# Optimization experiments

Measured on AMD Instinct MI355X. Metric: run time of the kernel, lower is better.

## Reference

```python
import jax, jax.numpy as jnp
import numpy as np

SLEN, BSZ, D_MODEL, N_HEAD, D_HEAD, PROJ_DIM = 2048, 2, 1024, 16, 64, 256
LN_EPS = 1e-5
PRIME_EPS = 1e-4


def setup_inputs() -> dict:
    key = jax.random.key(0)
    ks = jax.random.split(key, 4)
    h = jax.random.normal(ks[0], (SLEN, BSZ, D_MODEL), jnp.float32)
    W_qkvb = jax.random.normal(ks[1], (D_MODEL, N_HEAD * (3 * D_HEAD + 1)), jnp.float32) * (D_MODEL ** -0.5)
    W_o = jax.random.normal(ks[2], (N_HEAD * D_HEAD, D_MODEL), jnp.float32) * ((N_HEAD * D_HEAD) ** -0.5)
    ln_gamma = jnp.ones((D_MODEL,), jnp.float32)
    ln_beta = jnp.zeros((D_MODEL,), jnp.float32)
    # orthogonal random matrix (d_head, proj_dim): blocks of orthonormal cols, rows scaled to norm sqrt(d)
    rng = np.random.default_rng(0)
    blocks = []
    for _ in range(PROJ_DIM // D_HEAD):
        qm, _ = np.linalg.qr(rng.standard_normal((D_HEAD, D_HEAD)))
        blocks.append(qm)
    pm = np.concatenate(blocks, axis=1) * np.sqrt(D_HEAD)
    proj_matrix = jnp.asarray(pm, jnp.float32)  # (d_head, proj_dim)
    return {"h": h, "W_qkvb": W_qkvb, "W_o": W_o, "ln_gamma": ln_gamma,
            "ln_beta": ln_beta, "proj_matrix": proj_matrix}


def prime(x, pm):
    # FAVOR+ hyperbolic softmax-kernel features. x: (B,H,L,d), pm: (d,m) -> (B,H,L,2m)
    d = x.shape[-1]
    m = pm.shape[-1]
    xn = x * (d ** -0.25)
    proj = jnp.einsum('bhld,dm->bhlm', xn, pm)
    hnorm = 0.5 * jnp.sum(xn * xn, axis=-1, keepdims=True)
    feat = jnp.concatenate([jnp.exp(proj - hnorm), jnp.exp(-proj - hnorm)], axis=-1)
    return ((2 * m) ** -0.5) * (feat + PRIME_EPS)


def layer_norm(x, gamma, beta):
    mu = jnp.mean(x, axis=-1, keepdims=True)
    var = jnp.mean(jnp.square(x - mu), axis=-1, keepdims=True)
    return (x - mu) * jax.lax.rsqrt(var + LN_EPS) * gamma + beta


def reference(h, W_qkvb, W_o, ln_gamma, ln_beta, proj_matrix):
    slen, bsz, _ = h.shape
    qkvb = (h @ W_qkvb).reshape(slen, bsz, N_HEAD, 3 * D_HEAD + 1)
    q, k, v, hb = jnp.split(qkvb, [D_HEAD, 2 * D_HEAD, 3 * D_HEAD], axis=-1)
    hb = jax.nn.sigmoid(hb)
    # (L,B,H,*) -> (B,H,L,*)
    q = q.transpose(1, 2, 0, 3)
    k = k.transpose(1, 2, 0, 3)
    v = v.transpose(1, 2, 0, 3)
    hb = hb.transpose(1, 2, 0, 3)
    qp = prime(q, proj_matrix)
    kp = prime(k, proj_matrix)
    kp = kp / kp.sum(-1, keepdims=True)
    qp = qp / qp.sum(-1, keepdims=True)
    # time-major for the scan: (L,B,H,*)
    qpT = qp.transpose(2, 0, 1, 3)
    kpT = kp.transpose(2, 0, 1, 3)
    vT = v.transpose(2, 0, 1, 3)
    hbT = hb.transpose(2, 0, 1, 3)
    W0 = jnp.zeros((bsz, N_HEAD, 2 * PROJ_DIM, D_HEAD), h.dtype)

    def step(W, inp):
        qt, kt, vt, bt = inp  # (B,H,2m),(B,H,2m),(B,H,d),(B,H,1)
        v_old = jnp.einsum('bhpd,bhp->bhd', W, kt)
        W = W + jnp.einsum('bhp,bhd->bhpd', kt, bt * (vt - v_old))
        out = jnp.einsum('bhpd,bhp->bhd', W, qt)
        return W, out

    _, outs = jax.lax.scan(step, W0, (qpT, kpT, vT, hbT))  # outs: (L,B,H,d)
    scale = D_HEAD ** -0.5
    layer_out = (scale * outs).reshape(slen, bsz, N_HEAD * D_HEAD)
    attn_out = layer_out @ W_o
    return layer_norm(h + attn_out, ln_gamma, ln_beta)
```

## Files before the change

### kernel.cpp

```cpp
#include <hip/hip_runtime.h>
#include <hip/hip_bf16.h>

#define LSEQ   2048
#define BSZN   2
#define DMODEL 1024
#define NHEAD  16
#define DH     64
#define MPROJ  256
#define PF     512
#define CHK    64
#define NCHK   32
#define BHN    32
#define NQKV   3088
#define NQPAD  3200

typedef __hip_bfloat16 bf16;
typedef short bf16x8 __attribute__((ext_vector_type(8)));
typedef float f32x4 __attribute__((ext_vector_type(4)));

#define MFMA(a, b, c) __builtin_amdgcn_mfma_f32_16x16x32_bf16(a, b, c, 0, 0, 0)

#define UNP(u, a, b) { a = __uint_as_float((unsigned)(u) << 16); b = __uint_as_float((unsigned)(u) & 0xffff0000u); }

static __device__ __forceinline__ float b2f(bf16 x) {
  unsigned short us = *(unsigned short*)&x;
  return __uint_as_float((unsigned)us << 16);
}
static __device__ __forceinline__ bf16 f2b(float x) { return __float2bfloat16(x); }
static __device__ __forceinline__ unsigned pkbf(float a, float b) {
  bf16 x = __float2bfloat16(a), y = __float2bfloat16(b);
  return ((unsigned)(*(unsigned short*)&y) << 16) | (unsigned)(*(unsigned short*)&x);
}

static __device__ __forceinline__ void gl_lds16(const void* gsrc, void* ldst) {
  __builtin_amdgcn_global_load_lds(
      (const __attribute__((address_space(1))) unsigned int*)gsrc,
      (__attribute__((address_space(3))) unsigned int*)ldst, 16, 0, 0);
}

#define MEMFENCE asm volatile("" ::: "memory")
#define WAITV(n) asm volatile("s_waitcnt vmcnt(" #n ")" ::: "memory")
#define WAITLGKM asm volatile("s_waitcnt lgkmcnt(0)" ::: "memory")
#define BARRIER() __builtin_amdgcn_s_barrier()

__global__ __launch_bounds__(256)
void k_cvth(const float* __restrict__ h, bf16* __restrict__ hbf)
{
  const int gt = blockIdx.x * 256 + threadIdx.x;
  const int r = gt >> 7, ug = gt & 127;
  const int grp = ug >> 3, u = ug & 7;
  const float4 f0 = *(const float4*)&h[(size_t)r * 1024 + grp * 64 + u * 8];
  const float4 f1 = *(const float4*)&h[(size_t)r * 1024 + grp * 64 + u * 8 + 4];
  uint4 o;
  o.x = pkbf(f0.x, f0.y); o.y = pkbf(f0.z, f0.w);
  o.z = pkbf(f1.x, f1.y); o.w = pkbf(f1.z, f1.w);
  *(uint4*)&hbf[(size_t)r * 1024 + grp * 64 + ((u ^ (r & 7)) << 3)] = o;
}

__global__ __launch_bounds__(256)
void k_cvtw(const float* __restrict__ W, bf16* __restrict__ WT, int nsrc)
{
  __shared__ float sT[64][65];
  const int tid = threadIdx.x;
  const int n0 = blockIdx.x * 64, k0 = blockIdx.y * 64;
#pragma unroll
  for (int j = 0; j < 16; j++) {
    const int e = j * 256 + tid;
    const int r = e >> 6, c = e & 63;
    sT[r][c] = (n0 + c < nsrc) ? W[(size_t)(k0 + r) * nsrc + n0 + c] : 0.f;
  }
  __syncthreads();
#pragma unroll
  for (int j = 0; j < 2; j++) {
    const int uid = j * 256 + tid;
    const int rp = uid >> 3, u = uid & 7;
    uint4 o;
    o.x = pkbf(sT[u * 8 + 0][rp], sT[u * 8 + 1][rp]);
    o.y = pkbf(sT[u * 8 + 2][rp], sT[u * 8 + 3][rp]);
    o.z = pkbf(sT[u * 8 + 4][rp], sT[u * 8 + 5][rp]);
    o.w = pkbf(sT[u * 8 + 6][rp], sT[u * 8 + 7][rp]);
    *(uint4*)&WT[(size_t)(n0 + rp) * 1024 + k0 + ((u ^ (rp & 7)) << 3)] = o;
  }
}

__global__ __launch_bounds__(256)
void k_cvtpm(const float* __restrict__ pm, bf16* __restrict__ pmThi,
             bf16* __restrict__ pmTlo)
{
  const int n = threadIdx.x;
  float v[64];
#pragma unroll
  for (int d = 0; d < 64; d++) v[d] = pm[d * MPROJ + n] * 0.35355339059327373f;
  const int key = n & 7;
#pragma unroll
  for (int u = 0; u < 8; u++) {
    unsigned hi[4], lo[4];
#pragma unroll
    for (int j = 0; j < 4; j++) {
      const float a = v[u * 8 + j * 2], b = v[u * 8 + j * 2 + 1];
      const bf16 ah = f2b(a), bh_ = f2b(b);
      const float ar = a - b2f(ah), br = b - b2f(bh_);
      hi[j] = ((unsigned)(*(const unsigned short*)&bh_) << 16) | (unsigned)(*(const unsigned short*)&ah);
      const bf16 al = f2b(ar), bl = f2b(br);
      lo[j] = ((unsigned)(*(const unsigned short*)&bl) << 16) | (unsigned)(*(const unsigned short*)&al);
    }
    *(uint4*)&pmThi[(size_t)n * 64 + ((u ^ key) << 3)] = make_uint4(hi[0], hi[1], hi[2], hi[3]);
    *(uint4*)&pmTlo[(size_t)n * 64 + ((u ^ key) << 3)] = make_uint4(lo[0], lo[1], lo[2], lo[3]);
  }
}

#define GEMM_STAGE(Abase, Bbase, kt, b) {                                      \
  const size_t kb = (size_t)(kt) * 128;           \
  _Pragma("unroll")                                                            \
  for (int j = 0; j < 4; j++) {                                                \
    const int row = (w * 4 + j) * 8 + (lane >> 3);                             \
    gl_lds16((const char*)(Abase) + (size_t)(m0 + row) * 2048 + kb + (lane & 7) * 16, \
             &sA[b][(w * 4 + j) * 1024]);                                      \
  }                                                                            \
  _Pragma("unroll")                                                            \
  for (int j = 0; j < 4; j++) {                                                \
    const int row = (w * 4 + j) * 8 + (lane >> 3);                             \
    gl_lds16((const char*)(Bbase) + (size_t)(n0 + row) * 2048 + kb + (lane & 7) * 16, \
             &sB[b][(w * 4 + j) * 1024]);                                      \
  } }

#define GEMM_COMPUTE(b) {                                                      \
  _Pragma("unroll")                                                            \
  for (int ks = 0; ks < 2; ks++) {                                             \
    bf16x8 af[4], bfr[4];                                                      \
    _Pragma("unroll")                                                          \
    for (int f = 0; f < 4; f++) {                                              \
      const int row = wm * 64 + f * 16 + l16;                                  \
      af[f] = *(const bf16x8*)&sA[b][row * 128 + (((ks * 4 + lg) ^ xs) << 4)]; \
    }                                                                          \
    _Pragma("unroll")                                                          \
    for (int f = 0; f < 4; f++) {                                              \
      const int row = wn * 64 + f * 16 + l16;                                  \
      bfr[f] = *(const bf16x8*)&sB[b][row * 128 + (((ks * 4 + lg) ^ xs) << 4)]; \
    }                                                                          \
    _Pragma("unroll")                                                          \
    for (int fm = 0; fm < 4; fm++)                                             \
      _Pragma("unroll")                                                        \
      for (int fn = 0; fn < 4; fn++)                                           \
        acc[fm][fn] = MFMA(af[fm], bfr[fn], acc[fm][fn]);                      \
  } }

#define GEMM_PREAMBLE                                                          \
  __shared__ __align__(16) char sA[2][16384];                                  \
  __shared__ __align__(16) char sB[2][16384];                                  \
  const int tid = threadIdx.x, w = tid >> 6, lane = tid & 63;                  \
  const int l16 = lane & 15, lg = lane >> 4;                                   \
  const int wm = w >> 1, wn = w & 1;                                           \
  const int m0 = blockIdx.y * 128, n0 = blockIdx.x * 128;                      \
  const int xs = l16 & 7;                                                      \
  f32x4 acc[4][4];                                                             \
  _Pragma("unroll")                                                            \
  for (int i = 0; i < 4; i++)                                                  \
    _Pragma("unroll")                                                          \
    for (int j = 0; j < 4; j++) acc[i][j] = (f32x4){0.f, 0.f, 0.f, 0.f};

__global__ __launch_bounds__(256, 2)
void k_gemm_qkvb(const bf16* __restrict__ A, const bf16* __restrict__ B,
                 bf16* __restrict__ qh, bf16* __restrict__ kh,
                 bf16* __restrict__ vh, float* __restrict__ bbuf)
{
  GEMM_PREAMBLE
  GEMM_STAGE(A, B, 0, 0);
  __syncthreads();
  for (int kt = 0; kt < 16; kt++) {
    const int b = kt & 1;
    if (kt < 15) GEMM_STAGE(A, B, kt + 1, b ^ 1);
    GEMM_COMPUTE(b);
    __syncthreads();
  }
#pragma unroll
  for (int fm = 0; fm < 4; fm++)
#pragma unroll
    for (int fn = 0; fn < 4; fn++)
#pragma unroll
      for (int reg = 0; reg < 4; reg++) {
        const int m = m0 + wm * 64 + fm * 16 + lg * 4 + reg;
        const int n = n0 + wn * 64 + fn * 16 + l16;
        if (n >= NQKV) continue;
        const float v = acc[fm][fn][reg];
        const int l = m >> 1, bidx = m & 1;
        const int hd = n / 193;
        const int rem = n - hd * 193;
        const int bhi = bidx * NHEAD + hd;
        const size_t o = ((size_t)bhi * LSEQ + l) * DH;
        if (rem < 64) {
          const int d = rem;
          qh[o + ((((d >> 3) ^ (l & 7)) << 3) | (d & 7))] = f2b(v);
        } else if (rem < 128) {
          const int d = rem - 64;
          kh[o + ((((d >> 3) ^ (l & 7)) << 3) | (d & 7))] = f2b(v);
        } else if (rem < 192) {
          vh[o + rem - 128] = f2b(v);
        } else {
          bbuf[(size_t)bhi * LSEQ + l] = 1.f / (1.f + __expf(-v));
        }
      }
}

__global__ __launch_bounds__(256, 2)
void k_gemm_out(const bf16* __restrict__ A, const bf16* __restrict__ B,
                const float* __restrict__ h, float* __restrict__ ao)
{
  GEMM_PREAMBLE
  GEMM_STAGE(A, B, 0, 0);
  __syncthreads();
  for (int kt = 0; kt < 16; kt++) {
    const int b = kt & 1;
    if (kt < 15) GEMM_STAGE(A, B, kt + 1, b ^ 1);
    GEMM_COMPUTE(b);
    __syncthreads();
  }
#pragma unroll
  for (int fm = 0; fm < 4; fm++)
#pragma unroll
    for (int fn = 0; fn < 4; fn++)
#pragma unroll
      for (int reg = 0; reg < 4; reg++) {
        const int m = m0 + wm * 64 + fm * 16 + lg * 4 + reg;
        const int n = n0 + wn * 64 + fn * 16 + l16;
        const size_t o = (size_t)m * DMODEL + n;
        ao[o] = acc[fm][fn][reg] + h[o];
      }
}

__global__ __launch_bounds__(256, 2)
void k_featm(const bf16* __restrict__ qh, const bf16* __restrict__ kh,
             const bf16* __restrict__ pmThi, const bf16* __restrict__ pmTlo,
             bf16* __restrict__ Qp, bf16* __restrict__ Kp)
{
  __shared__ __align__(16) char sPM[2][32768];
  __shared__ __align__(16) char sX[8192];

  const int tid = threadIdx.x, w = tid >> 6, lane = tid & 63;
  const int l16 = lane & 15, lg = lane >> 4;
  const int xs = l16 & 7;
  const int l0 = blockIdx.x * 64, bhi = blockIdx.y;

#pragma unroll
  for (int j = 0; j < 8; j++)
    gl_lds16((const char*)pmThi + (size_t)(w * 8 + j) * 1024 + lane * 16,
             &sPM[0][(w * 8 + j) * 1024]);
#pragma unroll
  for (int j = 0; j < 8; j++)
    gl_lds16((const char*)pmTlo + (size_t)(w * 8 + j) * 1024 + lane * 16,
             &sPM[1][(w * 8 + j) * 1024]);
  {
    const char* qb = (const char*)(qh + ((size_t)bhi * LSEQ + l0) * DH);
#pragma unroll
    for (int j = 0; j < 2; j++)
      gl_lds16(qb + (size_t)(w * 2 + j) * 1024 + lane * 16, &sX[(w * 2 + j) * 1024]);
  }
  MEMFENCE;
  WAITV(0); BARRIER();

  const int srow = w * 16 + l16;
  const size_t gsr = (size_t)bhi * LSEQ + l0 + srow;

  for (int wh = 0; wh < 2; wh++) {
    bf16* dst = wh ? Kp : Qp;

    float hn;
    {
      const char* xrow = &sX[srow * 128];
      const uint4 a0 = *(const uint4*)&xrow[lg * 32];
      const uint4 a1 = *(const uint4*)&xrow[lg * 32 + 16];
      float f0, f1, f2, f3, f4, f5, f6, f7, a = 0.f;
      UNP(a0.x, f0, f1); UNP(a0.y, f2, f3); UNP(a0.z, f4, f5); UNP(a0.w, f6, f7);
      a = fmaf(f0, f0, a); a = fmaf(f1, f1, a); a = fmaf(f2, f2, a); a = fmaf(f3, f3, a);
      a = fmaf(f4, f4, a); a = fmaf(f5, f5, a); a = fmaf(f6, f6, a); a = fmaf(f7, f7, a);
      UNP(a1.x, f0, f1); UNP(a1.y, f2, f3); UNP(a1.z, f4, f5); UNP(a1.w, f6, f7);
      a = fmaf(f0, f0, a); a = fmaf(f1, f1, a); a = fmaf(f2, f2, a); a = fmaf(f3, f3, a);
      a = fmaf(f4, f4, a); a = fmaf(f5, f5, a); a = fmaf(f6, f6, a); a = fmaf(f7, f7, a);
      a += __shfl_xor(a, 16); a += __shfl_xor(a, 32);
      hn = a * 0.0625f;
    }

    f32x4 acc[16];
#pragma unroll
    for (int i = 0; i < 16; i++) acc[i] = (f32x4){0.f, 0.f, 0.f, 0.f};
#pragma unroll
    for (int ks = 0; ks < 2; ks++) {
      const bf16x8 bx = *(const bf16x8*)&sX[srow * 128 + (((ks * 4 + lg) ^ xs) << 4)];
#pragma unroll
      for (int mt = 0; mt < 16; mt++) {
        const bf16x8 ah = *(const bf16x8*)&sPM[0][(mt * 16 + l16) * 128 + (((ks * 4 + lg) ^ xs) << 4)];
        acc[mt] = MFMA(ah, bx, acc[mt]);
        const bf16x8 al = *(const bf16x8*)&sPM[1][(mt * 16 + l16) * 128 + (((ks * 4 + lg) ^ xs) << 4)];
        acc[mt] = MFMA(al, bx, acc[mt]);
      }
    }

    if (wh == 0) {
      BARRIER();
      const char* kb = (const char*)(kh + ((size_t)bhi * LSEQ + l0) * DH);
#pragma unroll
      for (int j = 0; j < 2; j++)
        gl_lds16(kb + (size_t)(w * 2 + j) * 1024 + lane * 16, &sX[(w * 2 + j) * 1024]);
      MEMFENCE;
    }

    float ss = 0.f;
#pragma unroll
    for (int mt = 0; mt < 16; mt++)
#pragma unroll
      for (int r = 0; r < 4; r++) {
        const float p = acc[mt][r];
        ss += __expf(p - hn) + __expf(-p - hn);
      }
    ss += __shfl_xor(ss, 16); ss += __shfl_xor(ss, 32);
    const float D = ss + 0.0512f;
    const float cc = 1e-4f / D;
    const float eo = hn + __logf(D);

    const size_t gb = gsr * PF;
    const int half = (lg & 1) * 4;
    const int ub = lg >> 1;
#pragma unroll
    for (int mt = 0; mt < 16; mt++) {
      const float v0 = __expf(acc[mt][0] - eo) + cc;
      const float v1 = __expf(acc[mt][1] - eo) + cc;
      const float v2 = __expf(acc[mt][2] - eo) + cc;
      const float v3 = __expf(acc[mt][3] - eo) + cc;
      const float n0 = __expf(-acc[mt][0] - eo) + cc;
      const float n1 = __expf(-acc[mt][1] - eo) + cc;
      const float n2 = __expf(-acc[mt][2] - eo) + cc;
      const float n3 = __expf(-acc[mt][3] - eo) + cc;
      const int u = mt * 2 + ub;
      *(uint2*)&dst[gb + ((u ^ xs) << 3) + half] = make_uint2(pkbf(v0, v1), pkbf(v2, v3));
      *(uint2*)&dst[gb + (((u + 32) ^ xs) << 3) + half] = make_uint2(pkbf(n0, n1), pkbf(n2, n3));
      __builtin_amdgcn_sched_barrier(0);
    }

    if (wh == 0) { WAITV(32); BARRIER(); }
  }
}

__global__ __launch_bounds__(256, 2)
void k_sgsolve(const bf16* __restrict__ Kp, const bf16* __restrict__ Qp,
               const float* __restrict__ bbuf,
               bf16* __restrict__ Gl, bf16* __restrict__ Tm,
               bf16* __restrict__ KpT)
{
  __shared__ __align__(16) char bufK[2][8192];
  __shared__ __align__(16) char bufQ[2][8192];
  __shared__ float sS[CHK][65];
  __shared__ float sT[CHK][65];
  __shared__ float sBeta[CHK];

  const int tid = threadIdx.x, w = tid >> 6, lane = tid & 63;
  const int l16 = lane & 15, lg = lane >> 4;
  const int xs = l16 & 7;
  const int c = blockIdx.x, bhi = blockIdx.y;
  const size_t cb = ((size_t)bhi * LSEQ + (size_t)c * CHK) * PF;
  const size_t rowb = (size_t)bhi * LSEQ + (size_t)c * CHK;
  const size_t ktb = (((size_t)bhi * NCHK + c) * 512) * 64;
  const size_t sb = (((size_t)bhi * NCHK + c) * CHK) * CHK;

  if (tid < CHK) sBeta[tid] = bbuf[rowb + tid];

  f32x4 accS[4], accG[4];
#pragma unroll
  for (int i = 0; i < 4; i++) { accS[i] = (f32x4){0.f,0.f,0.f,0.f}; accG[i] = (f32x4){0.f,0.f,0.f,0.f}; }

#define SG_STAGE(win, b) {                                                     \
  _Pragma("unroll")                                                            \
  for (int j = 0; j < 2; j++) {                                                \
    const int row = w * 16 + j * 8 + (lane >> 3);                              \
    gl_lds16((const char*)(Kp + cb) + (size_t)row * 1024 + (size_t)(win) * 128 + (lane & 7) * 16, \
             &bufK[b][(w * 16 + j * 8) * 128]);                                \
  }                                                                            \
  _Pragma("unroll")                                                            \
  for (int j = 0; j < 2; j++) {                                                \
    const int row = w * 16 + j * 8 + (lane >> 3);                              \
    gl_lds16((const char*)(Qp + cb) + (size_t)row * 1024 + (size_t)(win) * 128 + (lane & 7) * 16, \
             &bufQ[b][(w * 16 + j * 8) * 128]);                                \
  } }

  SG_STAGE(0, 0);
  MEMFENCE;

  for (int win = 0; win < 8; win++) {
    const int b = win & 1;
    if (win < 7) { SG_STAGE(win + 1, b ^ 1); MEMFENCE; }
    if (win == 0)      { WAITV(4); }
    else if (win < 7)  { WAITV(6); }
    else               { WAITV(2); }
    BARRIER();

#pragma unroll
    for (int ks = 0; ks < 2; ks++) {
      const bf16x8 aK = *(const bf16x8*)&bufK[b][(16 * w + l16) * 128 + (((ks * 4 + lg) ^ xs) << 4)];
      const bf16x8 aQ = *(const bf16x8*)&bufQ[b][(16 * w + l16) * 128 + (((ks * 4 + lg) ^ xs) << 4)];
      bf16x8 bK[4];
#pragma unroll
      for (int nt = 0; nt < 4; nt++)
        bK[nt] = *(const bf16x8*)&bufK[b][(nt * 16 + l16) * 128 + (((ks * 4 + lg) ^ xs) << 4)];
#pragma unroll
      for (int nt = 0; nt < 4; nt++) {
        accS[nt] = MFMA(aK, bK[nt], accS[nt]);
        accG[nt] = MFMA(aQ, bK[nt], accG[nt]);
      }
    }

#pragma unroll
    for (int jj = 0; jj < 2; jj++) {
      const int idx = jj * 256 + tid;
      const int pl = idx >> 3, l8 = idx & 7;
      unsigned short v[8];
#pragma unroll
      for (int j = 0; j < 8; j++) {
        const int l = l8 * 8 + j;
        v[j] = *(const unsigned short*)&bufK[b][l * 128 + (((pl >> 3) ^ (l & 7)) << 4) + (pl & 7) * 2];
      }
      uint4 o;
      o.x = ((unsigned)v[1] << 16) | v[0];
      o.y = ((unsigned)v[3] << 16) | v[2];
      o.z = ((unsigned)v[5] << 16) | v[4];
      o.w = ((unsigned)v[7] << 16) | v[6];
      const int p = win * 64 + pl;
      *(uint4*)&KpT[ktb + (size_t)p * 64 + ((l8 ^ (p & 7)) << 3)] = o;
    }
    BARRIER();
  }
#undef SG_STAGE

#pragma unroll
  for (int nt = 0; nt < 4; nt++)
#pragma unroll
    for (int reg = 0; reg < 4; reg++) {
      const int ri = 16 * w + lg * 4 + reg;
      const int cj = nt * 16 + l16;
      sS[ri][cj] = accS[nt][reg];
      Gl[sb + ri * 64 + (((cj >> 3) ^ (ri & 7)) << 3) + (cj & 7)] =
          f2b((cj <= ri) ? accG[nt][reg] : 0.f);
    }
  __syncthreads();

  if (tid < CHK) {
    const int j = tid;
    for (int i = 0; i < CHK; i++) {
      float acc = (i == j) ? 1.f : 0.f;
      for (int k = 0; k < i; k++) acc = fmaf(-sS[i][k], sT[k][j], acc);
      sT[i][j] = sBeta[i] * acc;
    }
  }
  __syncthreads();
  for (int t = tid; t < CHK * CHK; t += 256) {
    const int r = t >> 6, ccj = t & 63;
    Tm[sb + r * 64 + (((ccj >> 3) ^ (r & 7)) << 3) + (ccj & 7)] = f2b(sT[r][ccj]);
  }
}

__global__ __launch_bounds__(256, 1)
void k_scan(const bf16* __restrict__ Kp, const bf16* __restrict__ Qp,
            const bf16* __restrict__ vh, const bf16* __restrict__ Tm,
            const bf16* __restrict__ Gl, const bf16* __restrict__ KpT,
            bf16* __restrict__ lobf)
{
  __shared__ __align__(16) char sb[2][65536];
  __shared__ __align__(16) char sWT[16384];
  __shared__ __align__(16) char sUT[2048];
  __shared__ __align__(16) char suP[2048];

  const int tid = threadIdx.x;
  const int w = tid >> 6, lane = tid & 63;
  const int l16 = lane & 15, lg = lane >> 4;
  const int bhi = blockIdx.x & 31, dq = blockIdx.x >> 5;
  const int bidx = bhi >> 4, hd = bhi & 15;
  const int xs = l16 & 7;
  const int trow = 16 * w + l16;

  for (int i = tid; i < 4096; i += 256) ((unsigned*)sWT)[i] = 0u;

  f32x4 Wacc[8];
#pragma unroll
  for (int i = 0; i < 8; i++) Wacc[i] = (f32x4){0.f, 0.f, 0.f, 0.f};

  const size_t bh_base = (size_t)bhi * LSEQ * PF;
  const size_t tg0 = ((size_t)bhi * NCHK) * 4096;
  const size_t kt0 = ((size_t)bhi * NCHK) * (512 * 64);

  {
    const char* g = (const char*)(Kp + bh_base);
#pragma unroll
    for (int j = 0; j < 16; j++)
      gl_lds16(g + (w * 16 + j) * 1024 + lane * 16, &sb[0][(w * 16 + j) * 1024]);
    const char* gt = (const char*)(KpT + kt0);
#pragma unroll
    for (int j = 0; j < 16; j++)
      gl_lds16(gt + (w * 16 + j) * 1024 + lane * 16, &sb[1][(w * 16 + j) * 1024]);
  }
  MEMFENCE;
  WAITLGKM; BARRIER();

  int cur = 0;
  for (int c = 0; c < NCHK; c++) {
    BARRIER();

    const size_t cb = bh_base + (size_t)c * CHK * PF;
    const bf16* TmC  = Tm + tg0 + (size_t)c * 4096;
    const bf16* GlC  = Gl + tg0 + (size_t)c * 4096;
    const char* QpC  = (const char*)(Qp + cb);
    const char* KpN  = (const char*)(Kp + cb + CHK * PF);
    const char* KpTN = (const char*)(KpT + kt0 + (size_t)(c + 1) * (512 * 64));

    const bf16* vp = vh + ((size_t)bhi * LSEQ + c * 64 + w * 16 + lg * 4) * 64 + dq * 16 + l16;
    const float v0 = b2f(vp[0]),   v1 = b2f(vp[64]);
    const float v2 = b2f(vp[128]), v3 = b2f(vp[192]);
    const bf16x8 tf0 = *(const bf16x8*)&TmC[trow * 64 + (((lg    ) ^ xs) << 3)];
    const bf16x8 tf1 = *(const bf16x8*)&TmC[trow * 64 + (((4 + lg) ^ xs) << 3)];
    const bf16x8 gf0 = *(const bf16x8*)&GlC[trow * 64 + (((lg    ) ^ xs) << 3)];
    const bf16x8 gf1 = *(const bf16x8*)&GlC[trow * 64 + (((4 + lg) ^ xs) << 3)];
    MEMFENCE;
    WAITV(24);

    f32x4 a0v = (f32x4){0.f,0.f,0.f,0.f}, a1v = (f32x4){0.f,0.f,0.f,0.f};
#pragma unroll
    for (int ks = 0; ks < 16; ks += 2) {
      const bf16x8 aa0 = *(const bf16x8*)&sb[cur][trow * 1024 + ((((ks    ) * 4 + lg) ^ xs) << 4)];
      const bf16x8 bb0 = *(const bf16x8*)&sWT[l16 * 1024 + ((((ks    ) * 4 + lg) ^ xs) << 4)];
      a0v = MFMA(aa0, bb0, a0v);
      const bf16x8 aa1 = *(const bf16x8*)&sb[cur][trow * 1024 + ((((ks + 1) * 4 + lg) ^ xs) << 4)];
      const bf16x8 bb1 = *(const bf16x8*)&sWT[l16 * 1024 + ((((ks + 1) * 4 + lg) ^ xs) << 4)];
      a1v = MFMA(aa1, bb1, a1v);
    }
    {
      const int l0r = 16 * w + lg * 4;
      const unsigned plo = pkbf(v0 - (a0v[0] + a1v[0]), v1 - (a0v[1] + a1v[1]));
      const unsigned phi = pkbf(v2 - (a0v[2] + a1v[2]), v3 - (a0v[3] + a1v[3]));
      *(uint2*)&suP[l16 * 128 + ((((l0r >> 3)) ^ xs) << 4) + (l0r & 7) * 2] = make_uint2(plo, phi);
    }
    WAITLGKM;
#pragma unroll
    for (int j = 0; j < 16; j++)
      gl_lds16(QpC + (w * 16 + j) * 1024 + lane * 16, &sb[cur][(w * 16 + j) * 1024]);
    MEMFENCE;
    BARRIER();

    WAITV(18);
    {
      f32x4 ua = (f32x4){0.f,0.f,0.f,0.f};
      ua = MFMA(tf0, *(const bf16x8*)&suP[l16 * 128 + (((    lg) ^ xs) << 4)], ua);
      ua = MFMA(tf1, *(const bf16x8*)&suP[l16 * 128 + (((4 + lg) ^ xs) << 4)], ua);
      const int l0r = 16 * w + lg * 4;
      *(uint2*)&sUT[l16 * 128 + ((((l0r >> 3)) ^ xs) << 4) + (l0r & 7) * 2] =
          make_uint2(pkbf(ua[0], ua[1]), pkbf(ua[2], ua[3]));
    }
    WAITLGKM; BARRIER();

    WAITV(24);
    {
      bf16x8 bu[2];
#pragma unroll
      for (int ks = 0; ks < 2; ks++)
        bu[ks] = *(const bf16x8*)&sUT[l16 * 128 + (((ks * 4 + lg) ^ xs) << 4)];
#pragma unroll
      for (int mt = 0; mt < 8; mt++) {
        const int p = w * 128 + mt * 16 + l16;
#pragma unroll
        for (int ks = 0; ks < 2; ks++) {
          const bf16x8 aa = *(const bf16x8*)&sb[cur ^ 1][p * 128 + (((ks * 4 + lg) ^ xs) << 4)];
          Wacc[mt] = MFMA(aa, bu[ks], Wacc[mt]);
        }
      }
    }
    WAITLGKM;
    if (c < NCHK - 1) {
#pragma unroll
      for (int j = 0; j < 16; j++)
        gl_lds16(KpN + (w * 16 + j) * 1024 + lane * 16, &sb[cur ^ 1][(w * 16 + j) * 1024]);
      MEMFENCE;
    }

    if (c < NCHK - 1) { WAITV(16); } else { WAITV(0); }
    f32x4 o0 = (f32x4){0.f,0.f,0.f,0.f}, o1 = (f32x4){0.f,0.f,0.f,0.f};
#pragma unroll
    for (int ks = 0; ks < 16; ks += 2) {
      const bf16x8 aa0 = *(const bf16x8*)&sb[cur][trow * 1024 + ((((ks    ) * 4 + lg) ^ xs) << 4)];
      const bf16x8 bb0 = *(const bf16x8*)&sWT[l16 * 1024 + ((((ks    ) * 4 + lg) ^ xs) << 4)];
      o0 = MFMA(aa0, bb0, o0);
      const bf16x8 aa1 = *(const bf16x8*)&sb[cur][trow * 1024 + ((((ks + 1) * 4 + lg) ^ xs) << 4)];
      const bf16x8 bb1 = *(const bf16x8*)&sWT[l16 * 1024 + ((((ks + 1) * 4 + lg) ^ xs) << 4)];
      o1 = MFMA(aa1, bb1, o1);
    }
    o0 = MFMA(gf0, *(const bf16x8*)&sUT[l16 * 128 + (((    lg) ^ xs) << 4)], o0);
    o1 = MFMA(gf1, *(const bf16x8*)&sUT[l16 * 128 + (((4 + lg) ^ xs) << 4)], o1);
    {
      const int colb = hd * 64 + dq * 16 + l16;
#pragma unroll
      for (int reg = 0; reg < 4; reg++) {
        const int l = c * 64 + 16 * w + lg * 4 + reg;
        const int r = l * BSZN + bidx;
        const int cp = (colb & ~63) | ((((colb >> 3) & 7) ^ (r & 7)) << 3) | (colb & 7);
        lobf[(size_t)r * DMODEL + cp] = f2b(0.125f * (o0[reg] + o1[reg]));
      }
    }
    WAITLGKM; BARRIER();

    if (c < NCHK - 1) {
#pragma unroll
      for (int j = 0; j < 16; j++)
        gl_lds16(KpTN + (w * 16 + j) * 1024 + lane * 16, &sb[cur][(w * 16 + j) * 1024]);
      MEMFENCE;
    }
#pragma unroll
    for (int mt = 0; mt < 8; mt++) {
      const int p0m = w * 128 + mt * 16 + lg * 4;
      *(uint2*)&sWT[l16 * 1024 + ((((p0m >> 3)) ^ xs) << 4) + (p0m & 7) * 2] =
          make_uint2(pkbf(Wacc[mt][0], Wacc[mt][1]), pkbf(Wacc[mt][2], Wacc[mt][3]));
    }
    WAITLGKM;
    cur ^= 1;
  }
}

__global__ __launch_bounds__(256)
void k_ln(const float* __restrict__ ao, const float* __restrict__ gamma,
          const float* __restrict__ beta, float* __restrict__ out)
{
  const int row = blockIdx.x;
  const int tid = threadIdx.x;
  __shared__ float r1[4], r2[4];
  const float4 v = *(const float4*)&ao[(size_t)row * DMODEL + tid * 4];
  float s1 = v.x + v.y + v.z + v.w;
  float s2 = v.x * v.x + v.y * v.y + v.z * v.z + v.w * v.w;
  for (int off = 32; off > 0; off >>= 1) {
    s1 += __shfl_down(s1, off);
    s2 += __shfl_down(s2, off);
  }
  if ((tid & 63) == 0) { r1[tid >> 6] = s1; r2[tid >> 6] = s2; }
  __syncthreads();
  const float ts1 = r1[0] + r1[1] + r1[2] + r1[3];
  const float ts2 = r2[0] + r2[1] + r2[2] + r2[3];
  const float mu = ts1 * (1.f / DMODEL);
  const float var = ts2 * (1.f / DMODEL) - mu * mu;
  const float rs = rsqrtf(var + 1e-5f);
  const float4 g = *(const float4*)&gamma[tid * 4];
  const float4 b = *(const float4*)&beta[tid * 4];
  float4 o;
  o.x = (v.x - mu) * rs * g.x + b.x;
  o.y = (v.y - mu) * rs * g.y + b.y;
  o.z = (v.z - mu) * rs * g.z + b.z;
  o.w = (v.w - mu) * rs * g.w + b.w;
  *(float4*)&out[(size_t)row * DMODEL + tid * 4] = o;
}

extern "C" void kernel_launch(void* const* d_in, const int* in_sizes, int n_in,
                              void* d_out, int out_size, void* d_ws, size_t ws_size,
                              hipStream_t stream)
{
  (void)in_sizes; (void)n_in; (void)out_size; (void)ws_size;
  const float* h   = (const float*)d_in[0];
  const float* Wq  = (const float*)d_in[1];
  const float* Wo  = (const float*)d_in[2];
  const float* gam = (const float*)d_in[3];
  const float* bet = (const float*)d_in[4];
  const float* pm  = (const float*)d_in[5];
  float* out = (float*)d_out;

  char* ws = (char*)d_ws;
  size_t off = 0;
  auto alloc = [&](size_t bytes) -> void* {
    void* p = ws + off;
    off += (bytes + 255) & ~(size_t)255;
    return p;
  };
  bf16*  vh  = (bf16*)alloc((size_t)BHN * LSEQ * DH * 2);
  float* bbf = (float*)alloc((size_t)BHN * LSEQ * 4);
  bf16*  Kp  = (bf16*)alloc((size_t)BHN * LSEQ * PF * 2);
  bf16*  Qp  = (bf16*)alloc((size_t)BHN * LSEQ * PF * 2);
  bf16*  Tm  = (bf16*)alloc((size_t)BHN * NCHK * CHK * CHK * 2);
  bf16*  Gll = (bf16*)alloc((size_t)BHN * NCHK * CHK * CHK * 2);
  char*  R   = (char*)alloc((size_t)BHN * NCHK * 512 * 64 * 2);
  bf16*  WoT = (bf16*)alloc((size_t)DMODEL * DMODEL * 2);
  bf16*  pmThi = (bf16*)alloc((size_t)MPROJ * 64 * 2);
  bf16*  pmTlo = (bf16*)alloc((size_t)MPROJ * 64 * 2);
  bf16*  qh  = (bf16*)R;
  bf16*  kh  = (bf16*)(R + (size_t)BHN * LSEQ * DH * 2);
  bf16*  hbf = (bf16*)(R + (size_t)2 * BHN * LSEQ * DH * 2);
  bf16*  WqT = (bf16*)(R + (size_t)3 * BHN * LSEQ * DH * 2);
  bf16*  KpT = (bf16*)R;
  float* ao  = (float*)R;
  bf16*  lobf = (bf16*)d_out;

  k_cvth     <<<dim3(2048),                       256, 0, stream>>>(h, hbf);
  k_cvtw     <<<dim3(NQPAD / 64, 16),             256, 0, stream>>>(Wq, WqT, NQKV);
  k_cvtw     <<<dim3(DMODEL / 64, 16),            256, 0, stream>>>(Wo, WoT, DMODEL);
  k_cvtpm    <<<dim3(1),                          256, 0, stream>>>(pm, pmThi, pmTlo);
  k_gemm_qkvb<<<dim3(NQPAD / 128, 4096 / 128),    256, 0, stream>>>(hbf, WqT, qh, kh, vh, bbf);
  k_featm    <<<dim3(LSEQ / 64, BHN),             256, 0, stream>>>(qh, kh, pmThi, pmTlo, Qp, Kp);
  k_sgsolve  <<<dim3(NCHK, BHN),                  256, 0, stream>>>(Kp, Qp, bbf, Gll, Tm, KpT);
  k_scan     <<<dim3(128),                        256, 0, stream>>>(Kp, Qp, vh, Tm, Gll, KpT, lobf);
  k_gemm_out <<<dim3(DMODEL / 128, 4096 / 128),   256, 0, stream>>>(lobf, WoT, h, ao);
  k_ln       <<<dim3(4096),                       256, 0, stream>>>(ao, gam, bet, out);
}
```

Measured before the change: 398.5 us.

## Split chunked scan across 8 waves with K-dimension halves and LDS partial reduction

The sequential chunk scan kernel now runs with 512 threads instead of 256. Each pair of waves splits the 512-wide feature dimension in half for the Kp·W and Qp·W products and combines partial sums through a small LDS buffer. The W-state update is split so each wave owns 64 feature rows, and the sW reads are kept in registers and reused for the Q product. This roughly halves per-wave MFMA and LDS work on the serial critical path per chunk, at the cost of extra barriers, an LDS reduction step, and idle half-waves during the small T/G solves.

```diff
diff --git a/kernel.cpp b/kernel.cpp
--- a/kernel.cpp
+++ b/kernel.cpp
@@ -456,49 +456,54 @@
   }
 }
 
-__global__ __launch_bounds__(256, 1)
+__global__ __launch_bounds__(512, 2)
 void k_scan(const bf16* __restrict__ Kp, const bf16* __restrict__ Qp,
             const bf16* __restrict__ vh, const bf16* __restrict__ Tm,
             const bf16* __restrict__ Gl, const bf16* __restrict__ KpT,
             bf16* __restrict__ lobf)
 {
-  __shared__ __align__(16) char sb[2][65536];
+  __shared__ __align__(16) char bufA[65536];
+  __shared__ __align__(16) char bufB[65536];
   __shared__ __align__(16) char sWT[16384];
+  __shared__ __align__(16) char suP[2048];
   __shared__ __align__(16) char sUT[2048];
-  __shared__ __align__(16) char suP[2048];
+  __shared__ __align__(16) float pbuf[4][16][16];
 
   const int tid = threadIdx.x;
   const int w = tid >> 6, lane = tid & 63;
   const int l16 = lane & 15, lg = lane >> 4;
+  const int wp = w >> 1, h = w & 1;
   const int bhi = blockIdx.x & 31, dq = blockIdx.x >> 5;
   const int bidx = bhi >> 4, hd = bhi & 15;
   const int xs = l16 & 7;
-  const int trow = 16 * w + l16;
-
-  for (int i = tid; i < 4096; i += 256) ((unsigned*)sWT)[i] = 0u;
-
-  f32x4 Wacc[8];
-#pragma unroll
-  for (int i = 0; i < 8; i++) Wacc[i] = (f32x4){0.f, 0.f, 0.f, 0.f};
+
+  char* RA = bufA + w * 8192;
+  char* RB = bufB + w * 8192;
+
+  for (int i = tid; i < 4096; i += 512) ((unsigned*)sWT)[i] = 0u;
+
+  f32x4 Wacc[4];
+#pragma unroll
+  for (int i = 0; i < 4; i++) Wacc[i] = (f32x4){0.f, 0.f, 0.f, 0.f};
 
   const size_t bh_base = (size_t)bhi * LSEQ * PF;
   const size_t tg0 = ((size_t)bhi * NCHK) * 4096;
   const size_t kt0 = ((size_t)bhi * NCHK) * (512 * 64);
 
   {
+    const char* gt = (const char*)(KpT + kt0);
+#pragma unroll
+    for (int j = 0; j < 8; j++)
+      gl_lds16(gt + (size_t)w * 8192 + j * 1024 + lane * 16, RB + j * 1024);
     const char* g = (const char*)(Kp + bh_base);
 #pragma unroll
-    for (int j = 0; j < 16; j++)
-      gl_lds16(g + (w * 16 + j) * 1024 + lane * 16, &sb[0][(w * 16 + j) * 1024]);
-    const char* gt = (const char*)(KpT + kt0);
-#pragma unroll
-    for (int j = 0; j < 16; j++)
-      gl_lds16(gt + (w * 16 + j) * 1024 + lane * 16, &sb[1][(w * 16 + j) * 1024]);
+    for (int j = 0; j < 8; j++)
+      gl_lds16(g + (size_t)(16 * wp + 2 * j + (lane >> 5)) * 1024 + h * 512 + (lane & 31) * 16,
+               RA + j * 1024);
   }
   MEMFENCE;
-  WAITLGKM; BARRIER();
-
-  int cur = 0;
+  WAITV(0); WAITLGKM; BARRIER();
+
   for (int c = 0; c < NCHK; c++) {
     BARRIER();
 
@@ -508,114 +513,139 @@
     const char* QpC  = (const char*)(Qp + cb);
     const char* KpN  = (const char*)(Kp + cb + CHK * PF);
     const char* KpTN = (const char*)(KpT + kt0 + (size_t)(c + 1) * (512 * 64));
-
-    const bf16* vp = vh + ((size_t)bhi * LSEQ + c * 64 + w * 16 + lg * 4) * 64 + dq * 16 + l16;
-    const float v0 = b2f(vp[0]),   v1 = b2f(vp[64]);
-    const float v2 = b2f(vp[128]), v3 = b2f(vp[192]);
-    const bf16x8 tf0 = *(const bf16x8*)&TmC[trow * 64 + (((lg    ) ^ xs) << 3)];
-    const bf16x8 tf1 = *(const bf16x8*)&TmC[trow * 64 + (((4 + lg) ^ xs) << 3)];
-    const bf16x8 gf0 = *(const bf16x8*)&GlC[trow * 64 + (((lg    ) ^ xs) << 3)];
-    const bf16x8 gf1 = *(const bf16x8*)&GlC[trow * 64 + (((4 + lg) ^ xs) << 3)];
+    const int trow = 16 * wp + l16;
+
+    float v0 = 0.f, v1 = 0.f, v2 = 0.f, v3 = 0.f;
+    bf16x8 tf0 = {}, tf1 = {}, gf0 = {}, gf1 = {};
+    if (!h) {
+      const bf16* vp = vh + ((size_t)bhi * LSEQ + c * 64 + wp * 16 + lg * 4) * 64 + dq * 16 + l16;
+      v0 = b2f(vp[0]);   v1 = b2f(vp[64]);
+      v2 = b2f(vp[128]); v3 = b2f(vp[192]);
+      tf0 = *(const bf16x8*)&TmC[trow * 64 + ((lg ^ xs) << 3)];
+      tf1 = *(const bf16x8*)&TmC[trow * 64 + (((4 + lg) ^ xs) << 3)];
+      gf0 = *(const bf16x8*)&GlC[trow * 64 + ((lg ^ xs) << 3)];
+      gf1 = *(const bf16x8*)&GlC[trow * 64 + (((4 + lg) ^ xs) << 3)];
+    }
     MEMFENCE;
-    WAITV(24);
+    if (!h) { WAITV(12); } else { WAITV(0); }
 
     f32x4 a0v = (f32x4){0.f,0.f,0.f,0.f}, a1v = (f32x4){0.f,0.f,0.f,0.f};
-#pragma unroll
-    for (int ks = 0; ks < 16; ks += 2) {
-      const bf16x8 aa0 = *(const bf16x8*)&sb[cur][trow * 1024 + ((((ks    ) * 4 + lg) ^ xs) << 4)];
-      const bf16x8 bb0 = *(const bf16x8*)&sWT[l16 * 1024 + ((((ks    ) * 4 + lg) ^ xs) << 4)];
-      a0v = MFMA(aa0, bb0, a0v);
-      const bf16x8 aa1 = *(const bf16x8*)&sb[cur][trow * 1024 + ((((ks + 1) * 4 + lg) ^ xs) << 4)];
-      const bf16x8 bb1 = *(const bf16x8*)&sWT[l16 * 1024 + ((((ks + 1) * 4 + lg) ^ xs) << 4)];
-      a1v = MFMA(aa1, bb1, a1v);
-    }
-    {
-      const int l0r = 16 * w + lg * 4;
-      const unsigned plo = pkbf(v0 - (a0v[0] + a1v[0]), v1 - (a0v[1] + a1v[1]));
-      const unsigned phi = pkbf(v2 - (a0v[2] + a1v[2]), v3 - (a0v[3] + a1v[3]));
-      *(uint2*)&suP[l16 * 128 + ((((l0r >> 3)) ^ xs) << 4) + (l0r & 7) * 2] = make_uint2(plo, phi);
+    bf16x8 wb[8];
+#pragma unroll
+    for (int ks = 0; ks < 8; ks += 2) {
+      const bf16x8 aa0 = *(const bf16x8*)&RA[l16 * 512 + (((ks * 4 + lg) ^ xs) << 4)];
+      wb[ks] = *(const bf16x8*)&sWT[l16 * 1024 + ((((h * 32 + ks * 4 + lg)) ^ xs) << 4)];
+      a0v = MFMA(aa0, wb[ks], a0v);
+      const bf16x8 aa1 = *(const bf16x8*)&RA[l16 * 512 + ((((ks + 1) * 4 + lg) ^ xs) << 4)];
+      wb[ks + 1] = *(const bf16x8*)&sWT[l16 * 1024 + ((((h * 32 + (ks + 1) * 4 + lg)) ^ xs) << 4)];
+      a1v = MFMA(aa1, wb[ks + 1], a1v);
+    }
+    if (h) {
+      float4 pv;
+      pv.x = a0v[0] + a1v[0]; pv.y = a0v[1] + a1v[1];
+      pv.z = a0v[2] + a1v[2]; pv.w = a0v[3] + a1v[3];
+      *(float4*)&pbuf[wp][l16][lg * 4] = pv;
     }
     WAITLGKM;
-#pragma unroll
-    for (int j = 0; j < 16; j++)
-      gl_lds16(QpC + (w * 16 + j) * 1024 + lane * 16, &sb[cur][(w * 16 + j) * 1024]);
+    BARRIER();
+
+#pragma unroll
+    for (int j = 0; j < 8; j++)
+      gl_lds16(QpC + (size_t)(16 * wp + 2 * j + (lane >> 5)) * 1024 + h * 512 + (lane & 31) * 16,
+               RA + j * 1024);
     MEMFENCE;
+
+    if (!h) {
+      WAITV(8);
+      const float4 po = *(const float4*)&pbuf[wp][l16][lg * 4];
+      const float u0 = v0 - (a0v[0] + a1v[0]) - po.x;
+      const float u1 = v1 - (a0v[1] + a1v[1]) - po.y;
+      const float u2 = v2 - (a0v[2] + a1v[2]) - po.z;
+      const float u3 = v3 - (a0v[3] + a1v[3]) - po.w;
+      const int l0r = 16 * wp + lg * 4;
+      *(uint2*)&suP[l16 * 128 + (((l0r >> 3) ^ xs) << 4) + (l0r & 7) * 2] =
+          make_uint2(pkbf(u0, u1), pkbf(u2, u3));
+    }
+    WAITLGKM;
     BARRIER();
 
-    WAITV(18);
-    {
+    if (!h) {
       f32x4 ua = (f32x4){0.f,0.f,0.f,0.f};
-      ua = MFMA(tf0, *(const bf16x8*)&suP[l16 * 128 + (((    lg) ^ xs) << 4)], ua);
+      ua = MFMA(tf0, *(const bf16x8*)&suP[l16 * 128 + ((lg ^ xs) << 4)], ua);
       ua = MFMA(tf1, *(const bf16x8*)&suP[l16 * 128 + (((4 + lg) ^ xs) << 4)], ua);
-      const int l0r = 16 * w + lg * 4;
-      *(uint2*)&sUT[l16 * 128 + ((((l0r >> 3)) ^ xs) << 4) + (l0r & 7) * 2] =
+      const int l0r = 16 * wp + lg * 4;
+      *(uint2*)&sUT[l16 * 128 + (((l0r >> 3) ^ xs) << 4) + (l0r & 7) * 2] =
           make_uint2(pkbf(ua[0], ua[1]), pkbf(ua[2], ua[3]));
     }
-    WAITLGKM; BARRIER();
-
-    WAITV(24);
-    {
-      bf16x8 bu[2];
-#pragma unroll
-      for (int ks = 0; ks < 2; ks++)
-        bu[ks] = *(const bf16x8*)&sUT[l16 * 128 + (((ks * 4 + lg) ^ xs) << 4)];
-#pragma unroll
-      for (int mt = 0; mt < 8; mt++) {
-        const int p = w * 128 + mt * 16 + l16;
-#pragma unroll
-        for (int ks = 0; ks < 2; ks++) {
-          const bf16x8 aa = *(const bf16x8*)&sb[cur ^ 1][p * 128 + (((ks * 4 + lg) ^ xs) << 4)];
-          Wacc[mt] = MFMA(aa, bu[ks], Wacc[mt]);
-        }
-      }
+    WAITLGKM;
+    BARRIER();
+
+    const bf16x8 bu0 = *(const bf16x8*)&sUT[l16 * 128 + ((lg ^ xs) << 4)];
+    const bf16x8 bu1 = *(const bf16x8*)&sUT[l16 * 128 + (((4 + lg) ^ xs) << 4)];
+#pragma unroll
+    for (int mt = 0; mt < 4; mt++) {
+      const int pr = mt * 16 + l16;
+      const bf16x8 ka0 = *(const bf16x8*)&RB[pr * 128 + ((lg ^ xs) << 4)];
+      Wacc[mt] = MFMA(ka0, bu0, Wacc[mt]);
+      const bf16x8 ka1 = *(const bf16x8*)&RB[pr * 128 + (((4 + lg) ^ xs) << 4)];
+      Wacc[mt] = MFMA(ka1, bu1, Wacc[mt]);
     }
     WAITLGKM;
     if (c < NCHK - 1) {
 #pragma unroll
-      for (int j = 0; j < 16; j++)
-        gl_lds16(KpN + (w * 16 + j) * 1024 + lane * 16, &sb[cur ^ 1][(w * 16 + j) * 1024]);
+      for (int j = 0; j < 8; j++)
+        gl_lds16(KpTN + (size_t)w * 8192 + j * 1024 + lane * 16, RB + j * 1024);
       MEMFENCE;
     }
-
-    if (c < NCHK - 1) { WAITV(16); } else { WAITV(0); }
+#pragma unroll
+    for (int mt = 0; mt < 4; mt++) {
+      const int p0m = w * 64 + mt * 16 + lg * 4;
+      *(uint2*)&sWT[l16 * 1024 + (((p0m >> 3) ^ xs) << 4) + (p0m & 7) * 2] =
+          make_uint2(pkbf(Wacc[mt][0], Wacc[mt][1]), pkbf(Wacc[mt][2], Wacc[mt][3]));
+    }
+
+    if (c < NCHK - 1) { WAITV(8); } else { WAITV(0); }
     f32x4 o0 = (f32x4){0.f,0.f,0.f,0.f}, o1 = (f32x4){0.f,0.f,0.f,0.f};
 #pragma unroll
-    for (int ks = 0; ks < 16; ks += 2) {
-      const bf16x8 aa0 = *(const bf16x8*)&sb[cur][trow * 1024 + ((((ks    ) * 4 + lg) ^ xs) << 4)];
-      const bf16x8 bb0 = *(const bf16x8*)&sWT[l16 * 1024 + ((((ks    ) * 4 + lg) ^ xs) << 4)];
-      o0 = MFMA(aa0, bb0, o0);
-      const bf16x8 aa1 = *(const bf16x8*)&sb[cur][trow * 1024 + ((((ks + 1) * 4 + lg) ^ xs) << 4)];
-      const bf16x8 bb1 = *(const bf16x8*)&sWT[l16 * 1024 + ((((ks + 1) * 4 + lg) ^ xs) << 4)];
-      o1 = MFMA(aa1, bb1, o1);
-    }
-    o0 = MFMA(gf0, *(const bf16x8*)&sUT[l16 * 128 + (((    lg) ^ xs) << 4)], o0);
-    o1 = MFMA(gf1, *(const bf16x8*)&sUT[l16 * 128 + (((4 + lg) ^ xs) << 4)], o1);
-    {
+    for (int ks = 0; ks < 8; ks += 2) {
+      const bf16x8 qa0 = *(const bf16x8*)&RA[l16 * 512 + (((ks * 4 + lg) ^ xs) << 4)];
+      o0 = MFMA(qa0, wb[ks], o0);
+      const bf16x8 qa1 = *(const bf16x8*)&RA[l16 * 512 + ((((ks + 1) * 4 + lg) ^ xs) << 4)];
+      o1 = MFMA(qa1, wb[ks + 1], o1);
+    }
+    WAITLGKM;
+    if (c < NCHK - 1) {
+#pragma unroll
+      for (int j = 0; j < 8; j++)
+        gl_lds16(KpN + (size_t)(16 * wp + 2 * j + (lane >> 5)) * 1024 + h * 512 + (lane & 31) * 16,
+                 RA + j * 1024);
+      MEMFENCE;
+    }
+    if (h) {
+      float4 pv;
+      pv.x = o0[0] + o1[0]; pv.y = o0[1] + o1[1];
+      pv.z = o0[2] + o1[2]; pv.w = o0[3] + o1[3];
+      *(float4*)&pbuf[wp][l16][lg * 4] = pv;
+    } else {
+      o0 = MFMA(gf0, bu0, o0);
+      o1 = MFMA(gf1, bu1, o1);
+    }
+    WAITLGKM;
+    BARRIER();
+
+    if (!h) {
+      const float4 po = *(const float4*)&pbuf[wp][l16][lg * 4];
+      const float pr4[4] = {po.x, po.y, po.z, po.w};
       const int colb = hd * 64 + dq * 16 + l16;
 #pragma unroll
       for (int reg = 0; reg < 4; reg++) {
-        const int l = c * 64 + 16 * w + lg * 4 + reg;
+        const int l = c * 64 + 16 * wp + lg * 4 + reg;
         const int r = l * BSZN + bidx;
         const int cp = (colb & ~63) | ((((colb >> 3) & 7) ^ (r & 7)) << 3) | (colb & 7);
-        lobf[(size_t)r * DMODEL + cp] = f2b(0.125f * (o0[reg] + o1[reg]));
+        lobf[(size_t)r * DMODEL + cp] = f2b(0.125f * (o0[reg] + o1[reg] + pr4[reg]));
       }
     }
-    WAITLGKM; BARRIER();
-
-    if (c < NCHK - 1) {
-#pragma unroll
-      for (int j = 0; j < 16; j++)
-        gl_lds16(KpTN + (w * 16 + j) * 1024 + lane * 16, &sb[cur][(w * 16 + j) * 1024]);
-      MEMFENCE;
-    }
-#pragma unroll
-    for (int mt = 0; mt < 8; mt++) {
-      const int p0m = w * 128 + mt * 16 + lg * 4;
-      *(uint2*)&sWT[l16 * 1024 + ((((p0m >> 3)) ^ xs) << 4) + (p0m & 7) * 2] =
-          make_uint2(pkbf(Wacc[mt][0], Wacc[mt][1]), pkbf(Wacc[mt][2], Wacc[mt][3]));
-    }
     WAITLGKM;
-    cur ^= 1;
   }
 }
 
@@ -695,7 +725,7 @@
   k_gemm_qkvb<<<dim3(NQPAD / 128, 4096 / 128),    256, 0, stream>>>(hbf, WqT, qh, kh, vh, bbf);
   k_featm    <<<dim3(LSEQ / 64, BHN),             256, 0, stream>>>(qh, kh, pmThi, pmTlo, Qp, Kp);
   k_sgsolve  <<<dim3(NCHK, BHN),                  256, 0, stream>>>(Kp, Qp, bbf, Gll, Tm, KpT);
-  k_scan     <<<dim3(128),                        256, 0, stream>>>(Kp, Qp, vh, Tm, Gll, KpT, lobf);
+  k_scan     <<<dim3(128),                        512, 0, stream>>>(Kp, Qp, vh, Tm, Gll, KpT, lobf);
   k_gemm_out <<<dim3(DMODEL / 128, 4096 / 128),   256, 0, stream>>>(lobf, WoT, h, ao);
   k_ln       <<<dim3(4096),                       256, 0, stream>>>(ao, gam, bet, out);
 }
```

After: 367.9 us. -7.7%, faster.
